# Kernel optimization log

Measured on AMD Instinct MI355X. Metric: run time of the kernel, lower is better.

Reference implementation:

```python
import jax, jax.numpy as jnp
import numpy as np
from jax import lax

DIM = 8            # per-head dim
GROUPS = 192       # 3 * heads, groups of the pointwise aggreg conv
EPS_ATT = 1e-15
EPS_BN = 1e-5


def conv1x1(x, w):
    # x: (B,C,H,W), w: (O,C)
    return jnp.einsum('bchw,oc->bohw', x, w)


def setup_inputs() -> dict:
    key = jax.random.key(0)
    ks = jax.random.split(key, 9)
    B, C, H, W = 4, 512, 64, 64
    td3 = 3 * 512  # 3 * total_dim = 1536
    return {
        'x':       jax.random.normal(ks[0], (B, C, H, W), jnp.float32),
        'w_qkv':   jax.random.normal(ks[1], (td3, C), jnp.float32) * 0.05,
        'w_dw':    jax.random.normal(ks[2], (td3, 1, 5, 5), jnp.float32) * 0.05,
        'w_pw':    jax.random.normal(ks[3], (GROUPS, 8, 8), jnp.float32) * 0.05,
        'w_proj':  jax.random.normal(ks[4], (512, 1024), jnp.float32) * 0.05,
        'bn_gamma': 1.0 + 0.1 * jax.random.normal(ks[5], (512,), jnp.float32),
        'bn_beta': 0.1 * jax.random.normal(ks[6], (512,), jnp.float32),
        'bn_mean': 0.1 * jax.random.normal(ks[7], (512,), jnp.float32),
        'bn_var':  0.5 + jax.random.uniform(ks[8], (512,), jnp.float32),
    }


def reference(x, w_qkv, w_dw, w_pw, w_proj, bn_gamma, bn_beta, bn_mean, bn_var):
    B, _, H, W = x.shape
    # qkv 1x1 conv (no norm / act)
    qkv = conv1x1(x, w_qkv)                      # (B,1536,H,W)
    # multi-scale aggreg branch: depthwise 5x5 then grouped 1x1
    y = lax.conv_general_dilated(
        qkv, w_dw, window_strides=(1, 1), padding=((2, 2), (2, 2)),
        feature_group_count=qkv.shape[1],
        dimension_numbers=('NCHW', 'OIHW', 'NCHW'))
    yg = y.reshape(B, GROUPS, 8, H, W)
    y = jnp.einsum('bgihw,goi->bgohw', yg, w_pw).reshape(B, -1, H, W)
    ms = jnp.concatenate([qkv, y], axis=1)       # (B,3072,H,W)

    # relu linear attention (fp32)
    N = H * W
    t = ms.astype(jnp.float32).reshape(B, -1, 3 * DIM, N)   # (B,128,24,N)
    q = jax.nn.relu(t[:, :, :DIM])               # (B,h,8,N)
    k = jax.nn.relu(t[:, :, DIM:2 * DIM])        # (B,h,8,N)
    v = t[:, :, 2 * DIM:]                        # (B,h,8,N)
    v = jnp.concatenate([v, jnp.ones_like(v[:, :, :1])], axis=2)  # (B,h,9,N)
    vk = jnp.einsum('bhdn,bhen->bhde', v, k)     # (B,h,9,8)
    out = jnp.einsum('bhde,bhen->bhdn', vk, q)   # (B,h,9,N)
    out = out[:, :, :DIM] / (out[:, :, DIM:] + EPS_ATT)
    out = out.reshape(B, -1, H, W).astype(ms.dtype)  # (B,1024,H,W)

    # proj 1x1 conv + BatchNorm2d (inference, running stats)
    p = conv1x1(out, w_proj)                     # (B,512,H,W)
    scale = (bn_gamma / jnp.sqrt(bn_var + EPS_BN))[None, :, None, None]
    shift = (bn_beta - bn_mean * bn_gamma / jnp.sqrt(bn_var + EPS_BN))[None, :, None, None]
    return p * scale + shift
```

## Files before the change

### kernel.cpp

```cpp
#include <hip/hip_runtime.h>
#include <cstddef>


#define NPIX 4096
#define TD3 1536

typedef _Float16 f16;
typedef __attribute__((ext_vector_type(8))) _Float16 v8h;
typedef __attribute__((ext_vector_type(4))) float v4f;
typedef unsigned short ushort_t;

#define GLL16(g, l) __builtin_amdgcn_global_load_lds(                         \
    (const __attribute__((address_space(1))) unsigned int*)(g),               \
    (__attribute__((address_space(3))) unsigned int*)(l), 16, 0, 0)

template <int SPLITB, int BN>
__global__ __launch_bounds__(256, 1) void gemm_f16(
    const f16* __restrict__ Ah, const f16* __restrict__ Al,
    const f16* __restrict__ Bh, const f16* __restrict__ Bl,
    float* __restrict__ C, int M, int N, int K,
    const float* __restrict__ bn_g, const float* __restrict__ bn_b,
    const float* __restrict__ bn_m, const float* __restrict__ bn_v)
{
    __shared__ f16 AsH[2][128 * 32];
    __shared__ f16 AsL[2][128 * 32];
    __shared__ f16 BsH[2][256 * 32];
    __shared__ f16 BsL[SPLITB ? 2 : 1][SPLITB ? 256 * 32 : 64];

    const int tid  = threadIdx.x;
    const int lane = tid & 63;
    const int w    = tid >> 6;
    const int wm   = w >> 1, wn = w & 1;
    const int mBase = blockIdx.y * 128, nBase = blockIdx.x * 256;
    Bh += (size_t)blockIdx.z * N * K;
    if (SPLITB) Bl += (size_t)blockIdx.z * N * K;
    C  += (size_t)blockIdx.z * M * N;

    int aOff[2], bOff[4];
    int ldsA[2], ldsB[4];
    #pragma unroll
    for (int p = 0; p < 2; ++p) {
        int phys = (w * 2 + p) * 1024 + lane * 16;
        int lgc  = phys ^ (((phys >> 7) & 3) << 4);
        int r  = lgc >> 6;
        int ci = (lgc & 63) >> 1;
        aOff[p] = (mBase + r) * K + ci;
        ldsA[p] = (w * 2 + p) * 512;
    }
    #pragma unroll
    for (int p = 0; p < 4; ++p) {
        int phys = (w * 4 + p) * 1024 + lane * 16;
        int lgc  = phys ^ (((phys >> 7) & 3) << 4);
        int r  = lgc >> 6;
        int ci = (lgc & 63) >> 1;
        bOff[p] = (nBase + r) * K + ci;
        ldsB[p] = (w * 4 + p) * 512;
    }

    const int kq = lane >> 4;
    const int rm = lane & 15;
    const int slot = kq ^ ((rm >> 1) & 3);

    v4f acc[4][8];
    #pragma unroll
    for (int i = 0; i < 4; ++i)
        #pragma unroll
        for (int j = 0; j < 8; ++j)
            acc[i][j] = (v4f){0.f, 0.f, 0.f, 0.f};

    const int KT = K >> 5;

    #pragma unroll
    for (int p = 0; p < 2; ++p) {
        GLL16(Ah + aOff[p], &AsH[0][ldsA[p]]);
        GLL16(Al + aOff[p], &AsL[0][ldsA[p]]);
    }
    #pragma unroll
    for (int p = 0; p < 4; ++p) {
        GLL16(Bh + bOff[p], &BsH[0][ldsB[p]]);
        if (SPLITB) GLL16(Bl + bOff[p], &BsL[0][ldsB[p]]);
    }
    __syncthreads();

    for (int kt = 0; kt < KT; ++kt) {
        const int cb = kt & 1, nb = cb ^ 1;
        if (kt + 1 < KT) {
            const int ko = (kt + 1) * 32;
            #pragma unroll
            for (int p = 0; p < 2; ++p) {
                GLL16(Ah + aOff[p] + ko, &AsH[nb][ldsA[p]]);
                GLL16(Al + aOff[p] + ko, &AsL[nb][ldsA[p]]);
            }
            #pragma unroll
            for (int p = 0; p < 4; ++p) {
                GLL16(Bh + bOff[p] + ko, &BsH[nb][ldsB[p]]);
                if (SPLITB) GLL16(Bl + bOff[p] + ko, &BsL[nb][ldsB[p]]);
            }
        }

        v8h ah[4], al[4];
        #pragma unroll
        for (int i = 0; i < 4; ++i) {
            int rowA = wm * 64 + i * 16 + rm;
            ah[i] = *(const v8h*)&AsH[cb][rowA * 32 + slot * 8];
            al[i] = *(const v8h*)&AsL[cb][rowA * 32 + slot * 8];
        }
        #pragma unroll
        for (int j = 0; j < 8; ++j) {
            int rowB = wn * 128 + j * 16 + rm;
            v8h bh = *(const v8h*)&BsH[cb][rowB * 32 + slot * 8];
            v8h bl;
            if (SPLITB)
                bl = *(const v8h*)&BsL[cb][rowB * 32 + slot * 8];
            #pragma unroll
            for (int i = 0; i < 4; ++i) {
                acc[i][j] = __builtin_amdgcn_mfma_f32_16x16x32_f16(
                    ah[i], bh, acc[i][j], 0, 0, 0);
                acc[i][j] = __builtin_amdgcn_mfma_f32_16x16x32_f16(
                    al[i], bh, acc[i][j], 0, 0, 0);
                if (SPLITB)
                    acc[i][j] = __builtin_amdgcn_mfma_f32_16x16x32_f16(
                        ah[i], bl, acc[i][j], 0, 0, 0);
            }
        }
        __syncthreads();
    }

    const int rq = lane >> 4, cn = lane & 15;
    #pragma unroll
    for (int i = 0; i < 4; ++i) {
        #pragma unroll
        for (int rg = 0; rg < 4; ++rg) {
            int row = mBase + wm * 64 + i * 16 + rq * 4 + rg;
            float sc = 1.f, sh = 0.f;
            if (BN) {
                sc = bn_g[row] * rsqrtf(bn_v[row] + 1e-5f);
                sh = bn_b[row] - bn_m[row] * sc;
            }
            #pragma unroll
            for (int j = 0; j < 8; ++j) {
                int col = nBase + wn * 128 + j * 16 + cn;
                float v = acc[i][j][rg];
                C[(size_t)row * N + col] = BN ? (v * sc + sh) : v;
            }
        }
    }
}

__global__ __launch_bounds__(256) void cvt_split2(
    const float* __restrict__ s1, f16* __restrict__ d1h, f16* __restrict__ d1l,
    int n4_1,
    const float* __restrict__ s2, f16* __restrict__ d2h, f16* __restrict__ d2l,
    int n4_2)
{
    int i = blockIdx.x * 256 + threadIdx.x;
    const float* src; f16* dh; f16* dl; int idx;
    if (i < n4_1) { src = s1; dh = d1h; dl = d1l; idx = i; }
    else if (i < n4_1 + n4_2) { src = s2; dh = d2h; dl = d2l; idx = i - n4_1; }
    else return;
    float4 f = ((const float4*)src)[idx];
    f16 h[4], l[4];
    float ff[4] = {f.x, f.y, f.z, f.w};
    #pragma unroll
    for (int q = 0; q < 4; ++q) {
        h[q] = (f16)ff[q];
        l[q] = (f16)(ff[q] - (float)h[q]);
    }
    *(uint2*)&dh[(size_t)idx * 4] = *(uint2*)h;
    *(uint2*)&dl[(size_t)idx * 4] = *(uint2*)l;
}

__global__ __launch_bounds__(256) void transp_split(
    const float* __restrict__ src, f16* __restrict__ dh, f16* __restrict__ dl)
{
    __shared__ float t[64][65];
    const int tid = threadIdx.x;
    const int n0 = blockIdx.x * 64, c0 = blockIdx.y * 64, b = blockIdx.z;

    const int row = tid >> 2;
    const int nn  = (tid & 3) * 16;
    const float* sp = src + ((size_t)b * 512 + c0 + row) * NPIX + n0 + nn;
    #pragma unroll
    for (int q = 0; q < 4; ++q) {
        float4 f = *(const float4*)(sp + q * 4);
        t[row][nn + q * 4 + 0] = f.x;
        t[row][nn + q * 4 + 1] = f.y;
        t[row][nn + q * 4 + 2] = f.z;
        t[row][nn + q * 4 + 3] = f.w;
    }
    __syncthreads();

    const int nrow = tid >> 2;
    const int cc   = (tid & 3) * 16;
    f16 h[16], l[16];
    #pragma unroll
    for (int q = 0; q < 16; ++q) {
        float f = t[cc + q][nrow];
        h[q] = (f16)f;
        l[q] = (f16)(f - (float)h[q]);
    }
    size_t di = ((size_t)b * NPIX + n0 + nrow) * 512 + c0 + cc;
    *(uint4*)&dh[di] = *(uint4*)&h[0];
    *(uint4*)&dh[di + 8] = *(uint4*)&h[8];
    *(uint4*)&dl[di] = *(uint4*)&l[0];
    *(uint4*)&dl[di + 8] = *(uint4*)&l[8];
}

__global__ __launch_bounds__(256) void dwpw(
    const float* __restrict__ qkv, const float* __restrict__ w_dw,
    const float* __restrict__ w_pw, float* __restrict__ y)
{
    __shared__ float tile[8][36][68];

    const int tid = threadIdx.x;
    const int g = blockIdx.y;
    const int b = blockIdx.z;
    const int h0 = blockIdx.x * 32;
    const size_t cbase = (size_t)b * TD3 + g * 8;

    for (int idx = tid; idx < 288; idx += 256) {
        int ch = idx / 36, r = idx - ch * 36;
        *(float2*)&tile[ch][r][0]  = (float2){0.f, 0.f};
        *(float2*)&tile[ch][r][66] = (float2){0.f, 0.f};
    }
    #pragma unroll
    for (int it = 0; it < 18; ++it) {
        int idx = tid + it * 256;
        int ch = idx / 576;
        int rem = idx - ch * 576;
        int r = rem >> 4, q = rem & 15;
        int gh = h0 + r - 2;
        float4 v = {0.f, 0.f, 0.f, 0.f};
        if (gh >= 0 && gh < 64)
            v = *(const float4*)&qkv[(cbase + ch) * NPIX + gh * 64 + q * 4];
        *(float2*)&tile[ch][r][2 + q * 4] = (float2){v.x, v.y};
        *(float2*)&tile[ch][r][4 + q * 4] = (float2){v.z, v.w};
    }
    __syncthreads();

    const int wc0 = (tid & 15) * 4;
    const int rp  = tid >> 4;

    float acc[8][8];
    #pragma unroll
    for (int o = 0; o < 8; ++o)
        #pragma unroll
        for (int p = 0; p < 8; ++p) acc[o][p] = 0.f;

    #pragma unroll
    for (int ch = 0; ch < 8; ++ch) {
        const float* wdg = w_dw + (size_t)(g * 8 + ch) * 25;
        float wdr[25];
        #pragma unroll
        for (int t = 0; t < 25; ++t) wdr[t] = wdg[t];
        float wpr[8];
        #pragma unroll
        for (int o = 0; o < 8; ++o) wpr[o] = w_pw[g * 64 + o * 8 + ch];

        float w[6][8];
        #pragma unroll
        for (int rr = 0; rr < 6; ++rr) {
            *(float4*)&w[rr][0] = *(const float4*)&tile[ch][rp * 2 + rr][wc0];
            *(float4*)&w[rr][4] = *(const float4*)&tile[ch][rp * 2 + rr][wc0 + 4];
        }

        float dwv[8];
        #pragma unroll
        for (int s = 0; s < 2; ++s)
            #pragma unroll
            for (int cc = 0; cc < 4; ++cc) {
                float sum = 0.f;
                #pragma unroll
                for (int di = 0; di < 5; ++di)
                    #pragma unroll
                    for (int dj = 0; dj < 5; ++dj)
                        sum = fmaf(w[s + di][cc + dj], wdr[di * 5 + dj], sum);
                dwv[s * 4 + cc] = sum;
            }
        #pragma unroll
        for (int o = 0; o < 8; ++o)
            #pragma unroll
            for (int p = 0; p < 8; ++p)
                acc[o][p] = fmaf(dwv[p], wpr[o], acc[o][p]);
    }

    #pragma unroll
    for (int o = 0; o < 8; ++o)
        #pragma unroll
        for (int s = 0; s < 2; ++s) {
            float4 v = {acc[o][s * 4 + 0], acc[o][s * 4 + 1],
                        acc[o][s * 4 + 2], acc[o][s * 4 + 3]};
            *(float4*)&y[(cbase + o) * NPIX + (h0 + rp * 2 + s) * 64 + wc0] = v;
        }
}

__global__ __launch_bounds__(256) void attn_stats(
    const float* __restrict__ qkv, const float* __restrict__ yy,
    float* __restrict__ vkout)
{
    const int h = blockIdx.x;
    const int b = blockIdx.y;
    const float* src = (h < 64)
        ? qkv + ((size_t)b * TD3 + h * 24) * NPIX
        : yy  + ((size_t)b * TD3 + (h - 64) * 24) * NPIX;

    float acc[9][8];
    #pragma unroll
    for (int d = 0; d < 9; ++d)
        #pragma unroll
        for (int e = 0; e < 8; ++e) acc[d][e] = 0.f;

    for (int n = threadIdx.x; n < NPIX; n += 256) {
        float kr[8], vv[8];
        #pragma unroll
        for (int e = 0; e < 8; ++e) kr[e] = fmaxf(src[(8 + e) * NPIX + n], 0.f);
        #pragma unroll
        for (int d = 0; d < 8; ++d) vv[d] = src[(16 + d) * NPIX + n];
        #pragma unroll
        for (int d = 0; d < 8; ++d)
            #pragma unroll
            for (int e = 0; e < 8; ++e) acc[d][e] = fmaf(vv[d], kr[e], acc[d][e]);
        #pragma unroll
        for (int e = 0; e < 8; ++e) acc[8][e] += kr[e];
    }

    __shared__ float part[4][72];
    const int lane = threadIdx.x & 63, wave = threadIdx.x >> 6;
    #pragma unroll
    for (int i = 0; i < 72; ++i) {
        float v = acc[i / 8][i % 8];
        #pragma unroll
        for (int off = 32; off; off >>= 1) v += __shfl_down(v, off, 64);
        if (lane == 0) part[wave][i] = v;
    }
    __syncthreads();
    if (threadIdx.x < 72) {
        float v = part[0][threadIdx.x] + part[1][threadIdx.x] +
                  part[2][threadIdx.x] + part[3][threadIdx.x];
        vkout[((size_t)b * 128 + h) * 72 + threadIdx.x] = v;
    }
}

__global__ __launch_bounds__(256) void attn_apply_t(
    const float* __restrict__ qkv, const float* __restrict__ yy,
    const float* __restrict__ vkin, f16* __restrict__ attout)
{
    const int h = blockIdx.y;
    const int b = blockIdx.z;
    const int n = blockIdx.x * 256 + threadIdx.x;

    __shared__ float vk[72];
    if (threadIdx.x < 72)
        vk[threadIdx.x] = vkin[((size_t)b * 128 + h) * 72 + threadIdx.x];
    __syncthreads();

    const float* src = (h < 64)
        ? qkv + ((size_t)b * TD3 + h * 24) * NPIX
        : yy  + ((size_t)b * TD3 + (h - 64) * 24) * NPIX;

    float qr[8];
    #pragma unroll
    for (int e = 0; e < 8; ++e) qr[e] = fmaxf(src[e * NPIX + n], 0.f);

    float den = 0.f;
    #pragma unroll
    for (int e = 0; e < 8; ++e) den = fmaf(vk[64 + e], qr[e], den);
    float inv = 1.f / (den + 1e-15f);

    f16 o[8];
    #pragma unroll
    for (int d = 0; d < 8; ++d) {
        float num = 0.f;
        #pragma unroll
        for (int e = 0; e < 8; ++e) num = fmaf(vk[d * 8 + e], qr[e], num);
        o[d] = (f16)(num * inv);
    }
    *(uint4*)&attout[((size_t)b * NPIX + n) * 1024 + h * 8] = *(uint4*)o;
}

extern "C" void kernel_launch(void* const* d_in, const int* in_sizes, int n_in,
                              void* d_out, int out_size, void* d_ws, size_t ws_size,
                              hipStream_t stream)
{
    (void)in_sizes; (void)n_in; (void)out_size; (void)ws_size;
    const float* x      = (const float*)d_in[0];
    const float* w_qkv  = (const float*)d_in[1];
    const float* w_dw   = (const float*)d_in[2];
    const float* w_pw   = (const float*)d_in[3];
    const float* w_proj = (const float*)d_in[4];
    const float* bn_g   = (const float*)d_in[5];
    const float* bn_b   = (const float*)d_in[6];
    const float* bn_m   = (const float*)d_in[7];
    const float* bn_v   = (const float*)d_in[8];
    float* out = (float*)d_out;

    char* ws = (char*)d_ws;
    float* qkv     = (float*)(ws);
    float* y       = (float*)(ws + 100663296);
    f16*   x_t_h   = (f16*)(ws + 201326592);
    f16*   x_t_l   = (f16*)(ws + 218103808);
    f16*   attout  = (f16*)(ws + 201326592);
    f16*   w_qkv_h = (f16*)(ws + 234881024);
    f16*   w_qkv_l = (f16*)(ws + 236453888);
    f16*   w_proj_h= (f16*)(ws + 238026752);
    f16*   w_proj_l= (f16*)(ws + 239075328);
    float* vk      = out;

    cvt_split2<<<1280, 256, 0, stream>>>(
        w_qkv, w_qkv_h, w_qkv_l, 196608,
        w_proj, w_proj_h, w_proj_l, 131072);
    transp_split<<<dim3(64, 8, 4), 256, 0, stream>>>(x, x_t_h, x_t_l);
    gemm_f16<1, 0><<<dim3(16, 12, 4), 256, 0, stream>>>(
        w_qkv_h, w_qkv_l, x_t_h, x_t_l, qkv, 1536, 4096, 512,
        nullptr, nullptr, nullptr, nullptr);
    dwpw<<<dim3(2, 192, 4), 256, 0, stream>>>(qkv, w_dw, w_pw, y);
    attn_stats<<<dim3(128, 4), 256, 0, stream>>>(qkv, y, vk);
    attn_apply_t<<<dim3(16, 128, 4), 256, 0, stream>>>(qkv, y, vk, attout);
    gemm_f16<0, 1><<<dim3(16, 4, 4), 256, 0, stream>>>(
        w_proj_h, w_proj_l, attout, nullptr, out, 512, 4096, 1024,
        bn_g, bn_b, bn_m, bn_v);
}
```

Baseline: 368.1 us.

## Split GEMM into specialized QKV/proj kernels with deeper prefetch and retiled QKV

Replaces the templated GEMM with two specialized kernels. Both now keep two stages in flight through explicit vmcnt waits and barriers, with the next stage issued after the LDS reads complete. The QKV GEMM is retiled to 192x128 blocks with a larger grid, and both kernels allow 2 blocks per CU. The aim is to hide global-to-LDS latency and raise occupancy, at the cost of more register pressure and hand-tuned wait counts that could be wrong.

Measured after the change: 324.7 us. 1.13x faster.

```diff
diff --git a/kernel.cpp b/kernel.cpp
--- a/kernel.cpp
+++ b/kernel.cpp
@@ -8,57 +8,168 @@
 typedef _Float16 f16;
 typedef __attribute__((ext_vector_type(8))) _Float16 v8h;
 typedef __attribute__((ext_vector_type(4))) float v4f;
-typedef unsigned short ushort_t;
 
 #define GLL16(g, l) __builtin_amdgcn_global_load_lds(                         \
     (const __attribute__((address_space(1))) unsigned int*)(g),               \
     (__attribute__((address_space(3))) unsigned int*)(l), 16, 0, 0)
 
-template <int SPLITB, int BN>
-__global__ __launch_bounds__(256, 1) void gemm_f16(
+#define WAIT_VM(n) asm volatile("s_waitcnt vmcnt(" #n ")" ::: "memory")
+#define WAIT_LGKM0() asm volatile("s_waitcnt lgkmcnt(0)" ::: "memory")
+#define SBAR() __builtin_amdgcn_s_barrier()
+#define SCHED() __builtin_amdgcn_sched_barrier(0)
+
+__global__ __launch_bounds__(256, 2) void gemm_qkv(
     const f16* __restrict__ Ah, const f16* __restrict__ Al,
     const f16* __restrict__ Bh, const f16* __restrict__ Bl,
-    float* __restrict__ C, int M, int N, int K,
+    float* __restrict__ C)
+{
+    const int N = 4096, K = 512, KT = 16;
+    __shared__ f16 AsH[2][192 * 32];
+    __shared__ f16 AsL[2][192 * 32];
+    __shared__ f16 BsH[2][128 * 32];
+    __shared__ f16 BsL[2][128 * 32];
+
+    const int tid = threadIdx.x;
+    const int lane = tid & 63;
+    const int w = tid >> 6;
+    const int wm = w >> 1, wn = w & 1;
+    const int mBase = blockIdx.y * 192, nBase = blockIdx.x * 128;
+    Bh += (size_t)blockIdx.z * N * K;
+    Bl += (size_t)blockIdx.z * N * K;
+    C  += (size_t)blockIdx.z * 1536 * N;
+
+    int aOff[3], ldsA[3], bOff[2], ldsB[2];
+    #pragma unroll
+    for (int p = 0; p < 3; ++p) {
+        int c = w * 3 + p;
+        int phys = c * 1024 + lane * 16;
+        int lgc = phys ^ (((phys >> 7) & 3) << 4);
+        aOff[p] = (mBase + (lgc >> 6)) * K + ((lgc & 63) >> 1);
+        ldsA[p] = c * 512;
+    }
+    #pragma unroll
+    for (int p = 0; p < 2; ++p) {
+        int c = w * 2 + p;
+        int phys = c * 1024 + lane * 16;
+        int lgc = phys ^ (((phys >> 7) & 3) << 4);
+        bOff[p] = (nBase + (lgc >> 6)) * K + ((lgc & 63) >> 1);
+        ldsB[p] = c * 512;
+    }
+
+    const int kq = lane >> 4, rm = lane & 15;
+    const int slot = kq ^ ((rm >> 1) & 3);
+
+    v4f acc[6][4];
+    #pragma unroll
+    for (int i = 0; i < 6; ++i)
+        #pragma unroll
+        for (int j = 0; j < 4; ++j)
+            acc[i][j] = (v4f){0.f, 0.f, 0.f, 0.f};
+
+    auto stage = [&](int kt, int s) {
+        const int ko = kt * 32;
+        #pragma unroll
+        for (int p = 0; p < 3; ++p) {
+            GLL16(Ah + aOff[p] + ko, &AsH[s][ldsA[p]]);
+            GLL16(Al + aOff[p] + ko, &AsL[s][ldsA[p]]);
+        }
+        #pragma unroll
+        for (int p = 0; p < 2; ++p) {
+            GLL16(Bh + bOff[p] + ko, &BsH[s][ldsB[p]]);
+            GLL16(Bl + bOff[p] + ko, &BsL[s][ldsB[p]]);
+        }
+    };
+    stage(0, 0);
+    stage(1, 1);
+
+    for (int kt = 0; kt < KT; ++kt) {
+        const int cs = kt & 1;
+        if (kt < KT - 1) { WAIT_VM(10); } else { WAIT_VM(0); }
+        SBAR(); SCHED();
+
+        v8h ah[6], al[6], bh[4], bl[4];
+        #pragma unroll
+        for (int i = 0; i < 6; ++i) {
+            int rA = (wm * 96 + i * 16 + rm) * 32 + slot * 8;
+            ah[i] = *(const v8h*)&AsH[cs][rA];
+            al[i] = *(const v8h*)&AsL[cs][rA];
+        }
+        #pragma unroll
+        for (int j = 0; j < 4; ++j) {
+            int rB = (wn * 64 + j * 16 + rm) * 32 + slot * 8;
+            bh[j] = *(const v8h*)&BsH[cs][rB];
+            bl[j] = *(const v8h*)&BsL[cs][rB];
+        }
+        WAIT_LGKM0(); SCHED();
+        SBAR(); SCHED();
+
+        if (kt + 2 < KT) stage(kt + 2, cs);
+        #pragma unroll
+        for (int i = 0; i < 6; ++i)
+            #pragma unroll
+            for (int j = 0; j < 4; ++j) {
+                acc[i][j] = __builtin_amdgcn_mfma_f32_16x16x32_f16(
+                    ah[i], bh[j], acc[i][j], 0, 0, 0);
+                acc[i][j] = __builtin_amdgcn_mfma_f32_16x16x32_f16(
+                    al[i], bh[j], acc[i][j], 0, 0, 0);
+                acc[i][j] = __builtin_amdgcn_mfma_f32_16x16x32_f16(
+                    ah[i], bl[j], acc[i][j], 0, 0, 0);
+            }
+        SCHED();
+    }
+
+    const int rq = lane >> 4, cn = lane & 15;
+    #pragma unroll
+    for (int i = 0; i < 6; ++i)
+        #pragma unroll
+        for (int rg = 0; rg < 4; ++rg) {
+            int row = mBase + wm * 96 + i * 16 + rq * 4 + rg;
+            #pragma unroll
+            for (int j = 0; j < 4; ++j) {
+                int col = nBase + wn * 64 + j * 16 + cn;
+                C[(size_t)row * N + col] = acc[i][j][rg];
+            }
+        }
+}
+
+__global__ __launch_bounds__(256, 2) void gemm_proj(
+    const f16* __restrict__ Ah, const f16* __restrict__ Al,
+    const f16* __restrict__ Bh, float* __restrict__ C,
     const float* __restrict__ bn_g, const float* __restrict__ bn_b,
     const float* __restrict__ bn_m, const float* __restrict__ bn_v)
 {
+    const int N = 4096, K = 1024, KT = 32;
     __shared__ f16 AsH[2][128 * 32];
     __shared__ f16 AsL[2][128 * 32];
     __shared__ f16 BsH[2][256 * 32];
-    __shared__ f16 BsL[SPLITB ? 2 : 1][SPLITB ? 256 * 32 : 64];
-
-    const int tid  = threadIdx.x;
+
+    const int tid = threadIdx.x;
     const int lane = tid & 63;
-    const int w    = tid >> 6;
-    const int wm   = w >> 1, wn = w & 1;
+    const int w = tid >> 6;
+    const int wm = w >> 1, wn = w & 1;
     const int mBase = blockIdx.y * 128, nBase = blockIdx.x * 256;
     Bh += (size_t)blockIdx.z * N * K;
-    if (SPLITB) Bl += (size_t)blockIdx.z * N * K;
-    C  += (size_t)blockIdx.z * M * N;
-
-    int aOff[2], bOff[4];
-    int ldsA[2], ldsB[4];
+    C  += (size_t)blockIdx.z * 512 * N;
+
+    int aOff[2], ldsA[2], bOff[4], ldsB[4];
     #pragma unroll
     for (int p = 0; p < 2; ++p) {
-        int phys = (w * 2 + p) * 1024 + lane * 16;
-        int lgc  = phys ^ (((phys >> 7) & 3) << 4);
-        int r  = lgc >> 6;
-        int ci = (lgc & 63) >> 1;
-        aOff[p] = (mBase + r) * K + ci;
-        ldsA[p] = (w * 2 + p) * 512;
+        int c = w * 2 + p;
+        int phys = c * 1024 + lane * 16;
+        int lgc = phys ^ (((phys >> 7) & 3) << 4);
+        aOff[p] = (mBase + (lgc >> 6)) * K + ((lgc & 63) >> 1);
+        ldsA[p] = c * 512;
     }
     #pragma unroll
     for (int p = 0; p < 4; ++p) {
-        int phys = (w * 4 + p) * 1024 + lane * 16;
-        int lgc  = phys ^ (((phys >> 7) & 3) << 4);
-        int r  = lgc >> 6;
-        int ci = (lgc & 63) >> 1;
-        bOff[p] = (nBase + r) * K + ci;
-        ldsB[p] = (w * 4 + p) * 512;
-    }
-
-    const int kq = lane >> 4;
-    const int rm = lane & 15;
+        int c = w * 4 + p;
+        int phys = c * 1024 + lane * 16;
+        int lgc = phys ^ (((phys >> 7) & 3) << 4);
+        bOff[p] = (nBase + (lgc >> 6)) * K + ((lgc & 63) >> 1);
+        ldsB[p] = c * 512;
+    }
+
+    const int kq = lane >> 4, rm = lane & 15;
     const int slot = kq ^ ((rm >> 1) & 3);
 
     v4f acc[4][8];
@@ -68,83 +179,68 @@
         for (int j = 0; j < 8; ++j)
             acc[i][j] = (v4f){0.f, 0.f, 0.f, 0.f};
 
-    const int KT = K >> 5;
-
-    #pragma unroll
-    for (int p = 0; p < 2; ++p) {
-        GLL16(Ah + aOff[p], &AsH[0][ldsA[p]]);
-        GLL16(Al + aOff[p], &AsL[0][ldsA[p]]);
-    }
-    #pragma unroll
-    for (int p = 0; p < 4; ++p) {
-        GLL16(Bh + bOff[p], &BsH[0][ldsB[p]]);
-        if (SPLITB) GLL16(Bl + bOff[p], &BsL[0][ldsB[p]]);
-    }
-    __syncthreads();
+    auto stage = [&](int kt, int s) {
+        const int ko = kt * 32;
+        #pragma unroll
+        for (int p = 0; p < 2; ++p) {
+            GLL16(Ah + aOff[p] + ko, &AsH[s][ldsA[p]]);
+            GLL16(Al + aOff[p] + ko, &AsL[s][ldsA[p]]);
+        }
+        #pragma unroll
+        for (int p = 0; p < 4; ++p)
+            GLL16(Bh + bOff[p] + ko, &BsH[s][ldsB[p]]);
+    };
+    stage(0, 0);
+    stage(1, 1);
 
     for (int kt = 0; kt < KT; ++kt) {
-        const int cb = kt & 1, nb = cb ^ 1;
-        if (kt + 1 < KT) {
-            const int ko = (kt + 1) * 32;
-            #pragma unroll
-            for (int p = 0; p < 2; ++p) {
-                GLL16(Ah + aOff[p] + ko, &AsH[nb][ldsA[p]]);
-                GLL16(Al + aOff[p] + ko, &AsL[nb][ldsA[p]]);
+        const int cs = kt & 1;
+        if (kt < KT - 1) { WAIT_VM(8); } else { WAIT_VM(0); }
+        SBAR(); SCHED();
+
+        v8h ah[4], al[4], bh[8];
+        #pragma unroll
+        for (int i = 0; i < 4; ++i) {
+            int rA = (wm * 64 + i * 16 + rm) * 32 + slot * 8;
+            ah[i] = *(const v8h*)&AsH[cs][rA];
+            al[i] = *(const v8h*)&AsL[cs][rA];
+        }
+        #pragma unroll
+        for (int j = 0; j < 8; ++j) {
+            int rB = (wn * 128 + j * 16 + rm) * 32 + slot * 8;
+            bh[j] = *(const v8h*)&BsH[cs][rB];
+        }
+        WAIT_LGKM0(); SCHED();
+        SBAR(); SCHED();
+
+        if (kt + 2 < KT) stage(kt + 2, cs);
+
+        #pragma unroll
+        for (int i = 0; i < 4; ++i)
+            #pragma unroll
+            for (int j = 0; j < 8; ++j) {
+                acc[i][j] = __builtin_amdgcn_mfma_f32_16x16x32_f16(
+                    ah[i], bh[j], acc[i][j], 0, 0, 0);
+                acc[i][j] = __builtin_amdgcn_mfma_f32_16x16x32_f16(
+                    al[i], bh[j], acc[i][j], 0, 0, 0);
             }
-            #pragma unroll
-            for (int p = 0; p < 4; ++p) {
-                GLL16(Bh + bOff[p] + ko, &BsH[nb][ldsB[p]]);
-                if (SPLITB) GLL16(Bl + bOff[p] + ko, &BsL[nb][ldsB[p]]);
-            }
-        }
-
-        v8h ah[4], al[4];
-        #pragma unroll
-        for (int i = 0; i < 4; ++i) {
-            int rowA = wm * 64 + i * 16 + rm;
-            ah[i] = *(const v8h*)&AsH[cb][rowA * 32 + slot * 8];
-            al[i] = *(const v8h*)&AsL[cb][rowA * 32 + slot * 8];
-        }
-        #pragma unroll
-        for (int j = 0; j < 8; ++j) {
-            int rowB = wn * 128 + j * 16 + rm;
-            v8h bh = *(const v8h*)&BsH[cb][rowB * 32 + slot * 8];
-            v8h bl;
-            if (SPLITB)
-                bl = *(const v8h*)&BsL[cb][rowB * 32 + slot * 8];
-            #pragma unroll
-            for (int i = 0; i < 4; ++i) {
-                acc[i][j] = __builtin_amdgcn_mfma_f32_16x16x32_f16(
-                    ah[i], bh, acc[i][j], 0, 0, 0);
-                acc[i][j] = __builtin_amdgcn_mfma_f32_16x16x32_f16(
-                    al[i], bh, acc[i][j], 0, 0, 0);
-                if (SPLITB)
-                    acc[i][j] = __builtin_amdgcn_mfma_f32_16x16x32_f16(
-                        ah[i], bl, acc[i][j], 0, 0, 0);
-            }
-        }
-        __syncthreads();
+        SCHED();
     }
 
     const int rq = lane >> 4, cn = lane & 15;
     #pragma unroll
-    for (int i = 0; i < 4; ++i) {
+    for (int i = 0; i < 4; ++i)
         #pragma unroll
         for (int rg = 0; rg < 4; ++rg) {
             int row = mBase + wm * 64 + i * 16 + rq * 4 + rg;
-            float sc = 1.f, sh = 0.f;
-            if (BN) {
-                sc = bn_g[row] * rsqrtf(bn_v[row] + 1e-5f);
-                sh = bn_b[row] - bn_m[row] * sc;
-            }
+            float sc = bn_g[row] * rsqrtf(bn_v[row] + 1e-5f);
+            float sh = bn_b[row] - bn_m[row] * sc;
             #pragma unroll
             for (int j = 0; j < 8; ++j) {
                 int col = nBase + wn * 128 + j * 16 + cn;
-                float v = acc[i][j][rg];
-                C[(size_t)row * N + col] = BN ? (v * sc + sh) : v;
+                C[(size_t)row * N + col] = acc[i][j][rg] * sc + sh;
             }
         }
-    }
 }
 
 __global__ __launch_bounds__(256) void cvt_split2(
@@ -410,13 +506,11 @@
         w_qkv, w_qkv_h, w_qkv_l, 196608,
         w_proj, w_proj_h, w_proj_l, 131072);
     transp_split<<<dim3(64, 8, 4), 256, 0, stream>>>(x, x_t_h, x_t_l);
-    gemm_f16<1, 0><<<dim3(16, 12, 4), 256, 0, stream>>>(
-        w_qkv_h, w_qkv_l, x_t_h, x_t_l, qkv, 1536, 4096, 512,
-        nullptr, nullptr, nullptr, nullptr);
+    gemm_qkv<<<dim3(32, 8, 4), 256, 0, stream>>>(
+        w_qkv_h, w_qkv_l, x_t_h, x_t_l, qkv);
     dwpw<<<dim3(2, 192, 4), 256, 0, stream>>>(qkv, w_dw, w_pw, y);
     attn_stats<<<dim3(128, 4), 256, 0, stream>>>(qkv, y, vk);
     attn_apply_t<<<dim3(16, 128, 4), 256, 0, stream>>>(qkv, y, vk, attout);
-    gemm_f16<0, 1><<<dim3(16, 4, 4), 256, 0, stream>>>(
-        w_proj_h, w_proj_l, attout, nullptr, out, 512, 4096, 1024,
-        bn_g, bn_b, bn_m, bn_v);
-}
+    gemm_proj<<<dim3(16, 4, 4), 256, 0, stream>>>(
+        w_proj_h, w_proj_l, attout, out, bn_g, bn_b, bn_m, bn_v);
+}
```
